# Performance work log

Measured on AMD Instinct MI355X. Metric: run time of the kernel, lower is better.

## Reference

```python
import jax, jax.numpy as jnp
import numpy as np

N_JOINTS = 50
N_BONES = 50
# getSkeletalModelStructure() stand-in: 50 bones over 50 joints (i -> (i+1) % 50)
SRC = jnp.arange(N_BONES)
DST = (jnp.arange(N_BONES) + 1) % N_JOINTS
EPS = 1e-8


def _length_direct(x):
    # x: [B, T, 150] -> lengths [B, T, 50], directions [B, T, 150]
    B, T, _ = x.shape
    joints = x.reshape(B, T, N_JOINTS, 3)
    diff = joints[:, :, SRC, :] - joints[:, :, DST, :]      # [B, T, 50, 3]
    length = jnp.sqrt(jnp.sum(diff * diff, axis=-1))        # [B, T, 50]
    direct = diff / (length[..., None] + EPS)               # [B, T, 50, 3]
    return length, direct.reshape(B, T, N_BONES * 3)


def setup_inputs() -> dict:
    key = jax.random.key(0)
    k1, k2 = jax.random.split(key)
    preds = jax.random.normal(k1, (128, 1024, 150), dtype=jnp.float32)
    targets = jax.random.normal(k2, (128, 1024, 150), dtype=jnp.float32)
    return {"preds": preds, "targets": targets}


def reference(preds, targets):
    target_pad = 0.0
    loss_mask = (targets != target_pad).astype(jnp.float32)
    preds_masked = preds * loss_mask
    targets_masked = targets * loss_mask
    _, pd = _length_direct(preds_masked)
    _, td = _length_direct(targets_masked)
    pd = pd * loss_mask[:, :, :150]
    td = td * loss_mask[:, :, :150]
    # criterion = L1 (mean), criterion_bone = MSE (mean); loss_scale = 1.0
    loss = jnp.mean(jnp.abs(preds_masked - targets_masked)) + 0.1 * jnp.mean((pd - td) ** 2)
    return loss
```

## Files before the change

kernel.cpp:

```cpp
#include <hip/hip_runtime.h>


#define ROW_F    150
#define ROWS_PW  8
#define SPAN_F   (ROWS_PW * ROW_F)
#define SPAN_F4  (SPAN_F / 4)
#define WAVES_PB 4
#define GRID     1024
#define TOTAL_WAVES (GRID * WAVES_PB)

__global__ __launch_bounds__(256, 4) void loss_kernel(
    const float* __restrict__ preds,
    const float* __restrict__ targets,
    float* __restrict__ out,
    int iters, float inv_count)
{
    const float EPS = 1e-8f;
    __shared__ float sp[WAVES_PB][SPAN_F];
    __shared__ float st[WAVES_PB][SPAN_F];
    __shared__ float wsum[WAVES_PB];

    const int tid  = threadIdx.x;
    const int lane = tid & 63;
    const int wid  = tid >> 6;

    const float4* gp4 = reinterpret_cast<const float4*>(preds);
    const float4* gt4 = reinterpret_cast<const float4*>(targets);
    float4* sp4 = reinterpret_cast<float4*>(sp[wid]);
    float4* st4 = reinterpret_cast<float4*>(st[wid]);

    const int g0 = lane, g1 = lane + 64, g2 = lane + 128, g3 = lane + 192, g4 = lane + 256;
    const bool w4 = (g4 < SPAN_F4);
    const int g4c = w4 ? g4 : (SPAN_F4 - 1);

    const int row = lane >> 3;
    const int seg = lane & 7;
    const int j0 = (seg < 2) ? seg * 7 : 14 + (seg - 2) * 6;
    const int j1 = (seg < 2) ? j0 + 7 : j0 + 6;

    float l1 = 0.0f, mse = 0.0f;

    const int wglobal = blockIdx.x * WAVES_PB + wid;

    size_t sb = (size_t)wglobal * SPAN_F4;
    float4 rp0 = gp4[sb + g0], rp1 = gp4[sb + g1], rp2 = gp4[sb + g2],
           rp3 = gp4[sb + g3], rp4 = gp4[sb + g4c];
    float4 rt0 = gt4[sb + g0], rt1 = gt4[sb + g1], rt2 = gt4[sb + g2],
           rt3 = gt4[sb + g3], rt4 = gt4[sb + g4c];

#define L1ACC(P, T) do {                                         \
        l1 += ((T).x != 0.0f) ? fabsf((P).x - (T).x) : 0.0f;     \
        l1 += ((T).y != 0.0f) ? fabsf((P).y - (T).y) : 0.0f;     \
        l1 += ((T).z != 0.0f) ? fabsf((P).z - (T).z) : 0.0f;     \
        l1 += ((T).w != 0.0f) ? fabsf((P).w - (T).w) : 0.0f;     \
    } while (0)

    for (int it = 0; it < iters; ++it) {
        sp4[g0] = rp0; st4[g0] = rt0;
        sp4[g1] = rp1; st4[g1] = rt1;
        sp4[g2] = rp2; st4[g2] = rt2;
        sp4[g3] = rp3; st4[g3] = rt3;
        if (w4) { sp4[g4] = rp4; st4[g4] = rt4; }

        L1ACC(rp0, rt0); L1ACC(rp1, rt1); L1ACC(rp2, rt2); L1ACC(rp3, rt3);
        if (w4) L1ACC(rp4, rt4);

        if (it + 1 < iters) {
            size_t nb = (size_t)(wglobal + (size_t)(it + 1) * TOTAL_WAVES) * SPAN_F4;
            rp0 = gp4[nb + g0]; rp1 = gp4[nb + g1]; rp2 = gp4[nb + g2];
            rp3 = gp4[nb + g3]; rp4 = gp4[nb + g4c];
            rt0 = gt4[nb + g0]; rt1 = gt4[nb + g1]; rt2 = gt4[nb + g2];
            rt3 = gt4[nb + g3]; rt4 = gt4[nb + g4c];
        }

        const float* rpb = &sp[wid][row * ROW_F];
        const float* rtb = &st[wid][row * ROW_F];

        float pmP[3], tmP[3];
#pragma unroll
        for (int c = 0; c < 3; ++c) {
            float t = rtb[3 * j0 + c];
            float p = rpb[3 * j0 + c];
            pmP[c] = (t != 0.0f) ? p : 0.0f;
            tmP[c] = t;
        }

        for (int b = j0; b < j1; ++b) {
            int jn = b + 1;
            if (jn == 50) jn = 0;
            float pmN[3], tmN[3];
#pragma unroll
            for (int c = 0; c < 3; ++c) {
                float t = rtb[3 * jn + c];
                float p = rpb[3 * jn + c];
                pmN[c] = (t != 0.0f) ? p : 0.0f;
                tmN[c] = t;
            }
            float dp[3], dt[3], lp = 0.0f, lt = 0.0f;
#pragma unroll
            for (int c = 0; c < 3; ++c) {
                dp[c] = pmP[c] - pmN[c];
                dt[c] = tmP[c] - tmN[c];
                lp += dp[c] * dp[c];
                lt += dt[c] * dt[c];
            }
            float ip = __builtin_amdgcn_rcpf(__builtin_amdgcn_sqrtf(lp) + EPS);
            float iq = __builtin_amdgcn_rcpf(__builtin_amdgcn_sqrtf(lt) + EPS);
#pragma unroll
            for (int c = 0; c < 3; ++c) {
                float d = dp[c] * ip - dt[c] * iq;
                d = (tmP[c] != 0.0f) ? d : 0.0f;
                mse += d * d;
            }
#pragma unroll
            for (int c = 0; c < 3; ++c) { pmP[c] = pmN[c]; tmP[c] = tmN[c]; }
        }
    }

    float part = (l1 + 0.1f * mse) * inv_count;
#pragma unroll
    for (int off = 32; off > 0; off >>= 1)
        part += __shfl_down(part, off, 64);

    if (lane == 0) wsum[wid] = part;
    __syncthreads();
    if (tid == 0) {
        atomicAdd(out, wsum[0] + wsum[1] + wsum[2] + wsum[3]);
    }
}

extern "C" void kernel_launch(void* const* d_in, const int* in_sizes, int n_in,
                              void* d_out, int out_size, void* d_ws, size_t ws_size,
                              hipStream_t stream)
{
    const float* preds   = (const float*)d_in[0];
    const float* targets = (const float*)d_in[1];
    float* out = (float*)d_out;

    hipMemsetAsync(out, 0, sizeof(float) * out_size, stream);

    int n_elems = in_sizes[0];
    int n_rows  = n_elems / ROW_F;
    int spans   = n_rows / ROWS_PW;
    float inv_count = 1.0f / (float)n_elems;

    int iters = spans / TOTAL_WAVES;
    loss_kernel<<<GRID, 256, 0, stream>>>(preds, targets, out, iters, inv_count);
}
```

Before: 174.0 us.

## Halve rows per wave, double grid, and compute L1 from shared-memory loads

Each wave now processes 4 rows per span instead of 8, the grid is doubled and launch bounds ask for 8 blocks per CU. Each row is handled by 16 lanes with 3–4 bones each. The L1 term is now accumulated from the joint values already read from LDS in the bone loop, instead of a separate pass over the prefetched registers. The aim is more parallelism and less register pressure so the latency-bound bone loop gets more waves in flight. The cost is more LDS use per CU and slightly more complex per-lane bookkeeping.

```diff
diff --git a/kernel.cpp b/kernel.cpp
--- a/kernel.cpp
+++ b/kernel.cpp
@@ -2,14 +2,14 @@
 
 
 #define ROW_F    150
-#define ROWS_PW  8
+#define ROWS_PW  4
 #define SPAN_F   (ROWS_PW * ROW_F)
 #define SPAN_F4  (SPAN_F / 4)
 #define WAVES_PB 4
-#define GRID     1024
+#define GRID     2048
 #define TOTAL_WAVES (GRID * WAVES_PB)
 
-__global__ __launch_bounds__(256, 4) void loss_kernel(
+__global__ __launch_bounds__(256, 8) void loss_kernel(
     const float* __restrict__ preds,
     const float* __restrict__ targets,
     float* __restrict__ out,
@@ -29,48 +29,32 @@
     float4* sp4 = reinterpret_cast<float4*>(sp[wid]);
     float4* st4 = reinterpret_cast<float4*>(st[wid]);
 
-    const int g0 = lane, g1 = lane + 64, g2 = lane + 128, g3 = lane + 192, g4 = lane + 256;
-    const bool w4 = (g4 < SPAN_F4);
-    const int g4c = w4 ? g4 : (SPAN_F4 - 1);
+    const int g0 = lane, g1 = lane + 64, g2 = lane + 128;
+    const bool w2 = (g2 < SPAN_F4);
+    const int g2c = w2 ? g2 : (SPAN_F4 - 1);
 
-    const int row = lane >> 3;
-    const int seg = lane & 7;
-    const int j0 = (seg < 2) ? seg * 7 : 14 + (seg - 2) * 6;
-    const int j1 = (seg < 2) ? j0 + 7 : j0 + 6;
+    const int row = lane >> 4;
+    const int seg = lane & 15;
+    const int j0 = (seg < 2) ? seg * 4 : 8 + (seg - 2) * 3;
+    const int j1 = j0 + ((seg < 2) ? 4 : 3);
 
     float l1 = 0.0f, mse = 0.0f;
 
     const int wglobal = blockIdx.x * WAVES_PB + wid;
 
     size_t sb = (size_t)wglobal * SPAN_F4;
-    float4 rp0 = gp4[sb + g0], rp1 = gp4[sb + g1], rp2 = gp4[sb + g2],
-           rp3 = gp4[sb + g3], rp4 = gp4[sb + g4c];
-    float4 rt0 = gt4[sb + g0], rt1 = gt4[sb + g1], rt2 = gt4[sb + g2],
-           rt3 = gt4[sb + g3], rt4 = gt4[sb + g4c];
-
-#define L1ACC(P, T) do {                                         \
-        l1 += ((T).x != 0.0f) ? fabsf((P).x - (T).x) : 0.0f;     \
-        l1 += ((T).y != 0.0f) ? fabsf((P).y - (T).y) : 0.0f;     \
-        l1 += ((T).z != 0.0f) ? fabsf((P).z - (T).z) : 0.0f;     \
-        l1 += ((T).w != 0.0f) ? fabsf((P).w - (T).w) : 0.0f;     \
-    } while (0)
+    float4 rp0 = gp4[sb + g0], rp1 = gp4[sb + g1], rp2 = gp4[sb + g2c];
+    float4 rt0 = gt4[sb + g0], rt1 = gt4[sb + g1], rt2 = gt4[sb + g2c];
 
     for (int it = 0; it < iters; ++it) {
         sp4[g0] = rp0; st4[g0] = rt0;
         sp4[g1] = rp1; st4[g1] = rt1;
-        sp4[g2] = rp2; st4[g2] = rt2;
-        sp4[g3] = rp3; st4[g3] = rt3;
-        if (w4) { sp4[g4] = rp4; st4[g4] = rt4; }
-
-        L1ACC(rp0, rt0); L1ACC(rp1, rt1); L1ACC(rp2, rt2); L1ACC(rp3, rt3);
-        if (w4) L1ACC(rp4, rt4);
+        if (w2) { sp4[g2] = rp2; st4[g2] = rt2; }
 
         if (it + 1 < iters) {
             size_t nb = (size_t)(wglobal + (size_t)(it + 1) * TOTAL_WAVES) * SPAN_F4;
-            rp0 = gp4[nb + g0]; rp1 = gp4[nb + g1]; rp2 = gp4[nb + g2];
-            rp3 = gp4[nb + g3]; rp4 = gp4[nb + g4c];
-            rt0 = gt4[nb + g0]; rt1 = gt4[nb + g1]; rt2 = gt4[nb + g2];
-            rt3 = gt4[nb + g3]; rt4 = gt4[nb + g4c];
+            rp0 = gp4[nb + g0]; rp1 = gp4[nb + g1]; rp2 = gp4[nb + g2c];
+            rt0 = gt4[nb + g0]; rt1 = gt4[nb + g1]; rt2 = gt4[nb + g2c];
         }
 
         const float* rpb = &sp[wid][row * ROW_F];
@@ -83,6 +67,7 @@
             float p = rpb[3 * j0 + c];
             pmP[c] = (t != 0.0f) ? p : 0.0f;
             tmP[c] = t;
+            l1 += fabsf(pmP[c] - tmP[c]);
         }
 
         for (int b = j0; b < j1; ++b) {
@@ -95,6 +80,10 @@
                 float p = rpb[3 * jn + c];
                 pmN[c] = (t != 0.0f) ? p : 0.0f;
                 tmN[c] = t;
+            }
+            if (jn < j1 && jn != 0) {
+#pragma unroll
+                for (int c = 0; c < 3; ++c) l1 += fabsf(pmN[c] - tmN[c]);
             }
             float dp[3], dt[3], lp = 0.0f, lt = 0.0f;
 #pragma unroll
```

New measurement: 179.1 us. 2.9% more time.
